# Kernel optimization log

Hardware: AMD Instinct MI355X
Metric: run time of the kernel (lower is better)

The kernel has to match this reference:

```python
import jax, jax.numpy as jnp
import numpy as np

N = 100000   # nodes
E = 1600000  # edges (avg degree 16)
D = 128      # in_dim


def setup_inputs() -> dict:
    key = jax.random.key(0)
    k = jax.random.split(key, 8)
    h = jax.random.normal(k[0], (N, D), dtype=jnp.float32)
    d = jax.random.uniform(k[1], (N,), dtype=jnp.float32)  # per-node degree norm (e.g. deg^-0.5)
    yes_no = jax.random.uniform(k[2], (E,), dtype=jnp.float32)
    gate_w = jax.random.normal(k[3], (1, 2 * D), dtype=jnp.float32) * (1.414 / np.sqrt(2 * D))
    gate_b = jnp.zeros((1,), dtype=jnp.float32)
    yes_weight = jax.random.uniform(k[4], (), dtype=jnp.float32)
    no_weight = jax.random.uniform(k[5], (), dtype=jnp.float32)
    src = jax.random.randint(k[6], (E,), 0, N, dtype=jnp.int64)
    dst = jax.random.randint(k[7], (E,), 0, N, dtype=jnp.int64)
    return {"h": h, "d": d, "yes_no": yes_no, "gate_w": gate_w, "gate_b": gate_b,
            "yes_weight": yes_weight, "no_weight": no_weight, "src": src, "dst": dst}


def reference(h, d, yes_no, gate_w, gate_b, yes_weight, no_weight, src, dst):
    n, dim = h.shape
    # gate(cat[h_dst, h_src]) == h_dst @ W[:, :D].T + h_src @ W[:, D:].T + b
    # project once per node, then gather per edge (avoids [E, 2D] concat)
    p_dst = h @ gate_w[0, :dim]  # [N]
    p_src = h @ gate_w[0, dim:]  # [N]
    g = jnp.tanh(p_dst[dst] + p_src[src] + gate_b[0])  # [E]
    yn = jnp.tanh(yes_no * yes_weight + (1.0 - yes_no) * no_weight)  # [E]
    e = (g + yn) * 0.5 * d[dst] * d[src]  # [E] (dropout p=0 -> identity)
    m = h[src] * e[:, None]  # [E, D] edge messages
    z = jax.ops.segment_sum(m, dst, num_segments=n)  # [N, D]
    return z
```

## Files before the change

kernel.cpp:

```cpp
#include <hip/hip_runtime.h>

#define D 128
#define CAP 64
#define NPB 250
#define NBMAX 512
#define EPB 2048
#define BCAP 5120

typedef unsigned short u16x8 __attribute__((ext_vector_type(8)));
typedef float          f32x8 __attribute__((ext_vector_type(8)));

__device__ __forceinline__ unsigned short f2bf(float x) {
    unsigned int u = __float_as_uint(x);
    u += 0x7FFFu + ((u >> 16) & 1u);
    return (unsigned short)(u >> 16);
}
__device__ __forceinline__ float bf2f(unsigned short b) {
    return __uint_as_float(((unsigned int)b) << 16);
}
__device__ __forceinline__ float fast_tanh(float x) {
    float e = __expf(2.0f * x);
    return 1.0f - 2.0f * __builtin_amdgcn_rcpf(e + 1.0f);
}

__global__ __launch_bounds__(256) void proj_kernel(const float* __restrict__ h,
                                                   const float* __restrict__ gw,
                                                   const float* __restrict__ dnorm,
                                                   float4* __restrict__ q,
                                                   unsigned short* __restrict__ hb,
                                                   unsigned int* __restrict__ tails,
                                                   int n_nodes) {
    if (blockIdx.x == 0) {
        tails[threadIdx.x] = 0u;
        tails[threadIdx.x + 256] = 0u;
    }
    int node = (int)((blockIdx.x * blockDim.x + threadIdx.x) >> 6);
    int lane = threadIdx.x & 63;
    if (node >= n_nodes) return;
    const float2* hr2 = (const float2*)(h + (size_t)node * D);
    const float2* gw2 = (const float2*)gw;
    float2 hv = hr2[lane];
    float2 wa = gw2[lane];
    float2 wb = gw2[lane + 64];
    ushort2 hvb = make_ushort2(f2bf(hv.x), f2bf(hv.y));
    *(ushort2*)(hb + (size_t)node * D + 2 * lane) = hvb;
    float s1 = hv.x * wa.x + hv.y * wa.y;
    float s2 = hv.x * wb.x + hv.y * wb.y;
    #pragma unroll
    for (int off = 32; off > 0; off >>= 1) {
        s1 += __shfl_down(s1, off, 64);
        s2 += __shfl_down(s2, off, 64);
    }
    if (lane == 0) q[node] = make_float4(s1, s2, dnorm[node], 0.0f);
}

__global__ __launch_bounds__(512) void bin_kernel(const float4* __restrict__ q,
                                                  const float* __restrict__ yes_no,
                                                  const int* __restrict__ src,
                                                  const int* __restrict__ dst,
                                                  const float* __restrict__ gate_b,
                                                  const float* __restrict__ yes_w,
                                                  const float* __restrict__ no_w,
                                                  unsigned int* __restrict__ tails,
                                                  unsigned long long* __restrict__ recs,
                                                  int n_edges, int nb) {
    __shared__ unsigned long long sorted[EPB];
    __shared__ unsigned int hist[NBMAX];
    __shared__ unsigned int sbuf[NBMAX];
    __shared__ unsigned int base[NBMAX];
    __shared__ unsigned int cursor[NBMAX];
    __shared__ unsigned int gbase[NBMAX];

    int tid = threadIdx.x;
    int e0 = blockIdx.x * EPB;
    int n = n_edges - e0;
    if (n > EPB) n = EPB;

    hist[tid] = 0u;
    __syncthreads();

    for (int j = tid; j < n; j += 512) {
        unsigned int d = (unsigned int)dst[e0 + j];
        atomicAdd(&hist[d / NPB], 1u);
    }
    __syncthreads();

    sbuf[tid] = hist[tid];
    __syncthreads();
    unsigned int* pa = sbuf;
    unsigned int* pb = gbase;
    #pragma unroll
    for (int s = 1; s < NBMAX; s <<= 1) {
        unsigned int v = pa[tid] + ((tid >= s) ? pa[tid - s] : 0u);
        pb[tid] = v;
        __syncthreads();
        unsigned int* t = pa; pa = pb; pb = t;
    }
    unsigned int ex = (tid == 0) ? 0u : pa[tid - 1];
    base[tid] = ex;
    cursor[tid] = ex;
    __syncthreads();

    float gb = gate_b[0];
    float yw = yes_w[0];
    float nw = no_w[0];

    for (int j = tid; j < n; j += 512) {
        int e = e0 + j;
        int dd = dst[e];
        int ss = src[e];
        float yn = yes_no[e];
        float4 qt = q[dd];
        float4 qs = q[ss];
        float g = fast_tanh(qt.x + qs.y + gb);
        float y = fast_tanh(yn * yw + (1.0f - yn) * nw);
        float ce = (g + y) * 0.5f * qt.z * qs.z;
        int qv = (int)rintf(ce * 8191.0f) + 8192;
        unsigned int w0 = ((unsigned int)ss << 15) | (unsigned int)qv;
        unsigned int bk = (unsigned int)dd / NPB;
        unsigned int pos = atomicAdd(&cursor[bk], 1u);
        sorted[pos] = ((unsigned long long)(unsigned int)dd << 32) | (unsigned long long)w0;
    }
    __syncthreads();

    gbase[tid] = (hist[tid] > 0u) ? atomicAdd(&tails[tid], hist[tid]) : 0u;
    __syncthreads();

    for (int j = tid; j < n; j += 512) {
        unsigned long long r = sorted[j];
        unsigned int bk = (unsigned int)(r >> 32) / NPB;
        unsigned int gpos = gbase[bk] + ((unsigned int)j - base[bk]);
        if (gpos < BCAP)
            __builtin_nontemporal_store(r, recs + (size_t)bk * BCAP + gpos);
    }
}

__global__ __launch_bounds__(256) void scatter_kernel(const unsigned int* __restrict__ tails,
                                                      const unsigned long long* __restrict__ recs,
                                                      int* __restrict__ cnt,
                                                      unsigned int* __restrict__ csr,
                                                      int n_nodes) {
    __shared__ unsigned int sw0[BCAP];
    __shared__ unsigned char snl[BCAP];
    __shared__ unsigned int hist2[256];
    __shared__ unsigned int sa[256];
    __shared__ unsigned int sb[256];
    __shared__ unsigned int rowbase[256];
    __shared__ unsigned int cursor2[256];

    int b = blockIdx.x;
    int tid = threadIdx.x;
    unsigned int nrec = tails[b];
    if (nrec > BCAP) nrec = BCAP;
    const unsigned long long* rb = recs + (size_t)b * BCAP;
    int node0 = b * NPB;

    hist2[tid] = 0u;
    __syncthreads();

    for (unsigned int j = tid; j < nrec; j += 256) {
        unsigned long long r = __builtin_nontemporal_load(rb + j);
        unsigned int nl = (unsigned int)(r >> 32) - (unsigned int)node0;
        atomicAdd(&hist2[nl], 1u);
    }
    __syncthreads();

    sa[tid] = hist2[tid];
    __syncthreads();
    unsigned int* pa = sa;
    unsigned int* pb = sb;
    #pragma unroll
    for (int s = 1; s < 256; s <<= 1) {
        unsigned int v = pa[tid] + ((tid >= s) ? pa[tid - s] : 0u);
        pb[tid] = v;
        __syncthreads();
        unsigned int* t = pa; pa = pb; pb = t;
    }
    unsigned int ex = (tid == 0) ? 0u : pa[tid - 1];
    rowbase[tid] = ex;
    cursor2[tid] = ex;
    __syncthreads();

    for (unsigned int j = tid; j < nrec; j += 256) {
        unsigned long long r = rb[j];
        unsigned int nl = (unsigned int)(r >> 32) - (unsigned int)node0;
        unsigned int pos = atomicAdd(&cursor2[nl], 1u);
        sw0[pos] = (unsigned int)r;
        snl[pos] = (unsigned char)nl;
    }
    __syncthreads();

    for (unsigned int j = tid; j < nrec; j += 256) {
        unsigned int nl = snl[j];
        unsigned int k = j - rowbase[nl];
        if (k < CAP)
            csr[(size_t)(node0 + (int)nl) * CAP + k] = sw0[j];
    }
    if (tid < NPB && node0 + tid < n_nodes)
        cnt[node0 + tid] = (int)hist2[tid];
}

__global__ __launch_bounds__(256) void gather_kernel(const unsigned short* __restrict__ hb,
                                                     const int* __restrict__ cnt,
                                                     const unsigned int* __restrict__ csr,
                                                     float4* __restrict__ z4,
                                                     int n_nodes) {
    int node = (int)((blockIdx.x * blockDim.x + threadIdx.x) >> 4);
    int lane = threadIdx.x & 15;
    if (node >= n_nodes) return;
    int n = cnt[node];
    if (n > CAP) n = CAP;
    const unsigned int* row = csr + (size_t)node * CAP;
    const unsigned short* hbl = hb + 8 * lane;
    f32x8 acc = (f32x8)0.0f;
    const float inv = 1.0f / 8191.0f;
    int k = 0;
    for (; k + 3 < n; k += 4) {
        unsigned int e0 = row[k], e1 = row[k + 1], e2 = row[k + 2], e3 = row[k + 3];
        float c0 = (float)((int)(e0 & 0x7fffu) - 8192) * inv;
        float c1 = (float)((int)(e1 & 0x7fffu) - 8192) * inv;
        float c2 = (float)((int)(e2 & 0x7fffu) - 8192) * inv;
        float c3 = (float)((int)(e3 & 0x7fffu) - 8192) * inv;
        u16x8 a = *(const u16x8*)(hbl + (size_t)(e0 >> 15) * D);
        u16x8 b = *(const u16x8*)(hbl + (size_t)(e1 >> 15) * D);
        u16x8 c = *(const u16x8*)(hbl + (size_t)(e2 >> 15) * D);
        u16x8 d = *(const u16x8*)(hbl + (size_t)(e3 >> 15) * D);
        #pragma unroll
        for (int j = 0; j < 8; ++j) {
            acc[j] += bf2f(a[j]) * c0 + bf2f(b[j]) * c1 + bf2f(c[j]) * c2 + bf2f(d[j]) * c3;
        }
    }
    for (; k < n; ++k) {
        unsigned int e0 = row[k];
        float c0 = (float)((int)(e0 & 0x7fffu) - 8192) * inv;
        u16x8 a = *(const u16x8*)(hbl + (size_t)(e0 >> 15) * D);
        #pragma unroll
        for (int j = 0; j < 8; ++j) acc[j] += bf2f(a[j]) * c0;
    }
    float4 lo = make_float4(acc[0], acc[1], acc[2], acc[3]);
    float4 hi = make_float4(acc[4], acc[5], acc[6], acc[7]);
    z4[(size_t)node * (D / 4) + 2 * lane]     = lo;
    z4[(size_t)node * (D / 4) + 2 * lane + 1] = hi;
}

extern "C" void kernel_launch(void* const* d_in, const int* in_sizes, int n_in,
                              void* d_out, int out_size, void* d_ws, size_t ws_size,
                              hipStream_t stream) {
    const float* h       = (const float*)d_in[0];
    const float* dnorm   = (const float*)d_in[1];
    const float* yes_no  = (const float*)d_in[2];
    const float* gate_w  = (const float*)d_in[3];
    const float* gate_b  = (const float*)d_in[4];
    const float* yes_w   = (const float*)d_in[5];
    const float* no_w    = (const float*)d_in[6];
    const int*   src     = (const int*)d_in[7];
    const int*   dst     = (const int*)d_in[8];

    int n_nodes = in_sizes[0] / D;
    int n_edges = in_sizes[2];
    int nb = (n_nodes + NPB - 1) / NPB;

    char* ws = (char*)d_ws;
    size_t off = 0;
    auto take = [&](size_t bytes) {
        void* ptr = ws + off;
        off += (bytes + 15) & ~(size_t)15;
        return ptr;
    };
    float4*             q     = (float4*)take((size_t)n_nodes * sizeof(float4));
    unsigned short*     hb    = (unsigned short*)take((size_t)n_nodes * D * sizeof(unsigned short));
    int*                cnt   = (int*)take((size_t)n_nodes * sizeof(int));
    unsigned int*       csr   = (unsigned int*)take((size_t)n_nodes * CAP * sizeof(unsigned int));
    unsigned int*       tails = (unsigned int*)take((size_t)NBMAX * sizeof(unsigned int));
    unsigned long long* recs  = (unsigned long long*)take((size_t)nb * BCAP * sizeof(unsigned long long));
    (void)ws_size;

    proj_kernel<<<(n_nodes + 3) / 4, 256, 0, stream>>>(h, gate_w, dnorm, q, hb, tails, n_nodes);

    bin_kernel<<<(n_edges + EPB - 1) / EPB, 512, 0, stream>>>(
        q, yes_no, src, dst, gate_b, yes_w, no_w, tails, recs, n_edges, nb);

    scatter_kernel<<<nb, 256, 0, stream>>>(tails, recs, cnt, csr, n_nodes);

    gather_kernel<<<(n_nodes + 15) / 16, 256, 0, stream>>>(
        hb, cnt, csr, (float4*)d_out, n_nodes);
}
```

Before: 255.1 us.

## Fuse per-bucket CSR scatter and gather into one kernel using LDS edge lists

Merges the scatter and gather kernels so each 250-node bucket sorts its edge records in shared memory and then aggregates rows straight from LDS. The global CSR/cnt arrays and their write/read round trip go away, along with one kernel launch, and the per-node CAP truncation is dropped. The cost is far less parallelism: only nb (~400) blocks of 512 threads do the gather, versus ~6250 blocks before, which can limit latency hiding on the bf16 row fetches.

```diff
diff --git a/kernel.cpp b/kernel.cpp
--- a/kernel.cpp
+++ b/kernel.cpp
@@ -1,7 +1,6 @@
 #include <hip/hip_runtime.h>
 
 #define D 128
-#define CAP 64
 #define NPB 250
 #define NBMAX 512
 #define EPB 2048
@@ -9,6 +8,7 @@
 
 typedef unsigned short u16x8 __attribute__((ext_vector_type(8)));
 typedef float          f32x8 __attribute__((ext_vector_type(8)));
+typedef float          f32x4 __attribute__((ext_vector_type(4)));
 
 __device__ __forceinline__ unsigned short f2bf(float x) {
     unsigned int u = __float_as_uint(x);
@@ -135,13 +135,12 @@
     }
 }
 
-__global__ __launch_bounds__(256) void scatter_kernel(const unsigned int* __restrict__ tails,
-                                                      const unsigned long long* __restrict__ recs,
-                                                      int* __restrict__ cnt,
-                                                      unsigned int* __restrict__ csr,
-                                                      int n_nodes) {
+__global__ __launch_bounds__(512) void gscat_kernel(const unsigned int* __restrict__ tails,
+                                                    const unsigned long long* __restrict__ recs,
+                                                    const unsigned short* __restrict__ hb,
+                                                    float* __restrict__ z,
+                                                    int n_nodes) {
     __shared__ unsigned int sw0[BCAP];
-    __shared__ unsigned char snl[BCAP];
     __shared__ unsigned int hist2[256];
     __shared__ unsigned int sa[256];
     __shared__ unsigned int sb[256];
@@ -155,92 +154,84 @@
     const unsigned long long* rb = recs + (size_t)b * BCAP;
     int node0 = b * NPB;
 
-    hist2[tid] = 0u;
-    __syncthreads();
-
-    for (unsigned int j = tid; j < nrec; j += 256) {
-        unsigned long long r = __builtin_nontemporal_load(rb + j);
+    if (tid < 256) hist2[tid] = 0u;
+    __syncthreads();
+
+    for (unsigned int j = tid; j < nrec; j += 512) {
+        unsigned long long r = rb[j];
         unsigned int nl = (unsigned int)(r >> 32) - (unsigned int)node0;
         atomicAdd(&hist2[nl], 1u);
     }
     __syncthreads();
 
-    sa[tid] = hist2[tid];
+    if (tid < 256) sa[tid] = hist2[tid];
     __syncthreads();
     unsigned int* pa = sa;
     unsigned int* pb = sb;
     #pragma unroll
     for (int s = 1; s < 256; s <<= 1) {
-        unsigned int v = pa[tid] + ((tid >= s) ? pa[tid - s] : 0u);
-        pb[tid] = v;
+        if (tid < 256) {
+            unsigned int v = pa[tid] + ((tid >= s) ? pa[tid - s] : 0u);
+            pb[tid] = v;
+        }
         __syncthreads();
         unsigned int* t = pa; pa = pb; pb = t;
     }
-    unsigned int ex = (tid == 0) ? 0u : pa[tid - 1];
-    rowbase[tid] = ex;
-    cursor2[tid] = ex;
-    __syncthreads();
-
-    for (unsigned int j = tid; j < nrec; j += 256) {
+    if (tid < 256) {
+        unsigned int ex = (tid == 0) ? 0u : pa[tid - 1];
+        rowbase[tid] = ex;
+        cursor2[tid] = ex;
+    }
+    __syncthreads();
+
+    for (unsigned int j = tid; j < nrec; j += 512) {
         unsigned long long r = rb[j];
         unsigned int nl = (unsigned int)(r >> 32) - (unsigned int)node0;
         unsigned int pos = atomicAdd(&cursor2[nl], 1u);
         sw0[pos] = (unsigned int)r;
-        snl[pos] = (unsigned char)nl;
-    }
-    __syncthreads();
-
-    for (unsigned int j = tid; j < nrec; j += 256) {
-        unsigned int nl = snl[j];
-        unsigned int k = j - rowbase[nl];
-        if (k < CAP)
-            csr[(size_t)(node0 + (int)nl) * CAP + k] = sw0[j];
-    }
-    if (tid < NPB && node0 + tid < n_nodes)
-        cnt[node0 + tid] = (int)hist2[tid];
-}
-
-__global__ __launch_bounds__(256) void gather_kernel(const unsigned short* __restrict__ hb,
-                                                     const int* __restrict__ cnt,
-                                                     const unsigned int* __restrict__ csr,
-                                                     float4* __restrict__ z4,
-                                                     int n_nodes) {
-    int node = (int)((blockIdx.x * blockDim.x + threadIdx.x) >> 4);
-    int lane = threadIdx.x & 15;
-    if (node >= n_nodes) return;
-    int n = cnt[node];
-    if (n > CAP) n = CAP;
-    const unsigned int* row = csr + (size_t)node * CAP;
+    }
+    __syncthreads();
+
+    int grp  = tid >> 4;
+    int lane = tid & 15;
     const unsigned short* hbl = hb + 8 * lane;
-    f32x8 acc = (f32x8)0.0f;
     const float inv = 1.0f / 8191.0f;
-    int k = 0;
-    for (; k + 3 < n; k += 4) {
-        unsigned int e0 = row[k], e1 = row[k + 1], e2 = row[k + 2], e3 = row[k + 3];
-        float c0 = (float)((int)(e0 & 0x7fffu) - 8192) * inv;
-        float c1 = (float)((int)(e1 & 0x7fffu) - 8192) * inv;
-        float c2 = (float)((int)(e2 & 0x7fffu) - 8192) * inv;
-        float c3 = (float)((int)(e3 & 0x7fffu) - 8192) * inv;
-        u16x8 a = *(const u16x8*)(hbl + (size_t)(e0 >> 15) * D);
-        u16x8 b = *(const u16x8*)(hbl + (size_t)(e1 >> 15) * D);
-        u16x8 c = *(const u16x8*)(hbl + (size_t)(e2 >> 15) * D);
-        u16x8 d = *(const u16x8*)(hbl + (size_t)(e3 >> 15) * D);
-        #pragma unroll
-        for (int j = 0; j < 8; ++j) {
-            acc[j] += bf2f(a[j]) * c0 + bf2f(b[j]) * c1 + bf2f(c[j]) * c2 + bf2f(d[j]) * c3;
+    for (int nl = grp; nl < NPB; nl += 32) {
+        int node = node0 + nl;
+        if (node >= n_nodes) break;
+        unsigned int base2 = rowbase[nl];
+        int n = (int)hist2[nl];
+        f32x8 acc = (f32x8)0.0f;
+        int k = 0;
+        for (; k + 3 < n; k += 4) {
+            unsigned int e0 = sw0[base2 + k],     e1 = sw0[base2 + k + 1];
+            unsigned int e2 = sw0[base2 + k + 2], e3 = sw0[base2 + k + 3];
+            float c0 = (float)((int)(e0 & 0x7fffu) - 8192) * inv;
+            float c1 = (float)((int)(e1 & 0x7fffu) - 8192) * inv;
+            float c2 = (float)((int)(e2 & 0x7fffu) - 8192) * inv;
+            float c3 = (float)((int)(e3 & 0x7fffu) - 8192) * inv;
+            u16x8 a = *(const u16x8*)(hbl + (size_t)(e0 >> 15) * D);
+            u16x8 bb = *(const u16x8*)(hbl + (size_t)(e1 >> 15) * D);
+            u16x8 c = *(const u16x8*)(hbl + (size_t)(e2 >> 15) * D);
+            u16x8 d = *(const u16x8*)(hbl + (size_t)(e3 >> 15) * D);
+            #pragma unroll
+            for (int j = 0; j < 8; ++j) {
+                acc[j] += bf2f(a[j]) * c0 + bf2f(bb[j]) * c1 + bf2f(c[j]) * c2 + bf2f(d[j]) * c3;
+            }
         }
-    }
-    for (; k < n; ++k) {
-        unsigned int e0 = row[k];
-        float c0 = (float)((int)(e0 & 0x7fffu) - 8192) * inv;
-        u16x8 a = *(const u16x8*)(hbl + (size_t)(e0 >> 15) * D);
-        #pragma unroll
-        for (int j = 0; j < 8; ++j) acc[j] += bf2f(a[j]) * c0;
-    }
-    float4 lo = make_float4(acc[0], acc[1], acc[2], acc[3]);
-    float4 hi = make_float4(acc[4], acc[5], acc[6], acc[7]);
-    z4[(size_t)node * (D / 4) + 2 * lane]     = lo;
-    z4[(size_t)node * (D / 4) + 2 * lane + 1] = hi;
+        for (; k < n; ++k) {
+            unsigned int e0 = sw0[base2 + k];
+            float c0 = (float)((int)(e0 & 0x7fffu) - 8192) * inv;
+            u16x8 a = *(const u16x8*)(hbl + (size_t)(e0 >> 15) * D);
+            #pragma unroll
+            for (int j = 0; j < 8; ++j) acc[j] += bf2f(a[j]) * c0;
+        }
+        f32x4 lo = { acc[0], acc[1], acc[2], acc[3] };
+        f32x4 hi = { acc[4], acc[5], acc[6], acc[7] };
+        f32x4* zp = (f32x4*)(z + (size_t)node * D + 8 * lane);
+        __builtin_nontemporal_store(lo, zp);
+        __builtin_nontemporal_store(hi, zp + 1);
+    }
 }
 
 extern "C" void kernel_launch(void* const* d_in, const int* in_sizes, int n_in,
@@ -269,8 +260,6 @@
     };
     float4*             q     = (float4*)take((size_t)n_nodes * sizeof(float4));
     unsigned short*     hb    = (unsigned short*)take((size_t)n_nodes * D * sizeof(unsigned short));
-    int*                cnt   = (int*)take((size_t)n_nodes * sizeof(int));
-    unsigned int*       csr   = (unsigned int*)take((size_t)n_nodes * CAP * sizeof(unsigned int));
     unsigned int*       tails = (unsigned int*)take((size_t)NBMAX * sizeof(unsigned int));
     unsigned long long* recs  = (unsigned long long*)take((size_t)nb * BCAP * sizeof(unsigned long long));
     (void)ws_size;
@@ -280,8 +269,5 @@
     bin_kernel<<<(n_edges + EPB - 1) / EPB, 512, 0, stream>>>(
         q, yes_no, src, dst, gate_b, yes_w, no_w, tails, recs, n_edges, nb);
 
-    scatter_kernel<<<nb, 256, 0, stream>>>(tails, recs, cnt, csr, n_nodes);
-
-    gather_kernel<<<(n_nodes + 15) / 16, 256, 0, stream>>>(
-        hb, cnt, csr, (float4*)d_out, n_nodes);
-}
+    gscat_kernel<<<nb, 512, 0, stream>>>(tails, recs, hb, (float*)d_out, n_nodes);
+}
```

Result: faster. 238.3 us (median of 2 runs) (-6.6%).
